# Kernel optimization log

Measured on AMD Instinct MI355X. Metric: run time of the kernel, lower is better.

The kernel has to match this reference:

```python
import jax, jax.numpy as jnp
import numpy as np
import math

EMB = 128
HW = 128

def setup_inputs() -> dict:
    key = jax.random.key(0)
    k_t, k1, k2, k3, k4 = jax.random.split(key, 5)
    B = 8192
    t = jax.random.uniform(k_t, (B,), dtype=jnp.float32)
    s = 1.0 / math.sqrt(EMB)
    W1 = jax.random.uniform(k1, (EMB, EMB), dtype=jnp.float32, minval=-s, maxval=s)
    b1 = jax.random.uniform(k2, (EMB,), dtype=jnp.float32, minval=-s, maxval=s)
    W2 = jax.random.uniform(k3, (EMB, EMB), dtype=jnp.float32, minval=-s, maxval=s)
    b2 = jax.random.uniform(k4, (EMB,), dtype=jnp.float32, minval=-s, maxval=s)
    return {"t": t, "W1": W1, "b1": b1, "W2": W2, "b2": b2}

def reference(t, W1, b1, W2, b2):
    # sinusoidal embedding: 64 log-spaced freqs in [1, 1000]
    freqs = jnp.exp(jnp.linspace(math.log(1.0), math.log(1000.0), EMB // 2)).astype(jnp.float32)
    ang = (2.0 * math.pi) * freqs  # [64]
    phase = t[:, None] * ang[None, :]  # [B, 64]
    emb = jnp.concatenate([jnp.sin(phase), jnp.cos(phase)], axis=-1)  # [B, 128]
    # MLP: Linear -> SiLU -> Linear -> SiLU (torch Linear: x @ W.T + b)
    h = jax.nn.silu(emb @ W1.T + b1)
    h = jax.nn.silu(h @ W2.T + b2)
    # [B,1,1,128] nearest-upsampled to [B,1,128,128]: broadcast along H
    out = jnp.broadcast_to(h[:, None, None, :], (h.shape[0], 1, HW, HW))
    return out
```

## Files before the change

### kernel.cpp

```cpp
#include <hip/hip_runtime.h>
#include <math.h>

typedef float f32x4 __attribute__((ext_vector_type(4)));

__global__ __launch_bounds__(256) void k_mlp(
    const float* __restrict__ t,
    const float* __restrict__ W1, const float* __restrict__ b1,
    const float* __restrict__ W2, const float* __restrict__ b2,
    float* __restrict__ hs)
{
    __shared__ __attribute__((aligned(16))) float emb[16][128];
    __shared__ __attribute__((aligned(16))) float h1[16][128];

    const int tid  = threadIdx.x;
    const int base = blockIdx.x * 16;

    #pragma unroll
    for (int i = 0; i < 4; ++i) {
        int idx = i * 256 + tid;
        int b   = idx >> 6;
        int k   = idx & 63;
        double a   = (double)k * (6.907755278982137 / 63.0);
        float freq = (float)exp(a);
        float ang  = 6.2831853071795865f * freq;
        float ph   = t[base + b] * ang;
        float sv, cv;
        sincosf(ph, &sv, &cv);
        emb[b][k]      = sv;
        emb[b][64 + k] = cv;
    }
    __syncthreads();

    const int jj   = tid & 127;
    const int half = tid >> 7;

    {
        float acc[8];
        float bv = b1[jj];
        #pragma unroll
        for (int m = 0; m < 8; ++m) acc[m] = bv;
        const float4* w = (const float4*)(W1 + jj * 128);
        #pragma unroll
        for (int k4 = 0; k4 < 32; ++k4) {
            float4 wv = w[k4];
            #pragma unroll
            for (int m = 0; m < 8; ++m) {
                float4 ev = ((const float4*)emb[half * 8 + m])[k4];
                acc[m] = fmaf(wv.x, ev.x, acc[m]);
                acc[m] = fmaf(wv.y, ev.y, acc[m]);
                acc[m] = fmaf(wv.z, ev.z, acc[m]);
                acc[m] = fmaf(wv.w, ev.w, acc[m]);
            }
        }
        #pragma unroll
        for (int m = 0; m < 8; ++m) {
            float a = acc[m];
            h1[half * 8 + m][jj] = a / (1.0f + expf(-a));
        }
    }
    __syncthreads();

    {
        float acc[8];
        float bv = b2[jj];
        #pragma unroll
        for (int m = 0; m < 8; ++m) acc[m] = bv;
        const float4* w = (const float4*)(W2 + jj * 128);
        #pragma unroll
        for (int k4 = 0; k4 < 32; ++k4) {
            float4 wv = w[k4];
            #pragma unroll
            for (int m = 0; m < 8; ++m) {
                float4 ev = ((const float4*)h1[half * 8 + m])[k4];
                acc[m] = fmaf(wv.x, ev.x, acc[m]);
                acc[m] = fmaf(wv.y, ev.y, acc[m]);
                acc[m] = fmaf(wv.z, ev.z, acc[m]);
                acc[m] = fmaf(wv.w, ev.w, acc[m]);
            }
        }
        #pragma unroll
        for (int m = 0; m < 8; ++m) {
            float a = acc[m];
            hs[(size_t)(base + half * 8 + m) * 128 + jj] = a / (1.0f + expf(-a));
        }
    }
}

__global__ __launch_bounds__(256) void k_bcast(
    const float* __restrict__ hs, float* __restrict__ out)
{
    const int tid = threadIdx.x;
    const size_t b = blockIdx.x;
    f32x4 v = ((const f32x4*)(hs + b * 128))[tid & 31];
    f32x4* d = (f32x4*)(out + b * 16384);
    #pragma unroll
    for (int c = 0; c < 16; ++c) {
        d[c * 256 + tid] = v;
    }
}

extern "C" void kernel_launch(void* const* d_in, const int* in_sizes, int n_in,
                              void* d_out, int out_size, void* d_ws, size_t ws_size,
                              hipStream_t stream) {
    const float* t  = (const float*)d_in[0];
    const float* W1 = (const float*)d_in[1];
    const float* b1 = (const float*)d_in[2];
    const float* W2 = (const float*)d_in[3];
    const float* b2 = (const float*)d_in[4];
    float* out = (float*)d_out;
    float* hs  = (float*)d_ws;
    const int B = in_sizes[0];

    k_mlp  <<<B / 16, 256, 0, stream>>>(t, W1, b1, W2, b2, hs);
    k_bcast<<<B,      256, 0, stream>>>(hs, out);
}
```

Measured before the change: 549.7 us.

## Fuse MLP and broadcast into one kernel with swizzled LDS-staged weights

Merges the MLP kernel and the broadcast kernel into a single kernel, so the intermediate hidden vectors stay in shared memory instead of making a round trip through a global workspace, and one launch is removed. Each block now handles 8 batch rows instead of 16. It stages each weight matrix transposed into a 64KB shared buffer using an XOR swizzle to avoid bank conflicts, replacing per-thread strided global weight reads. The cost is that every block reloads both 64KB weight matrices, and the large shared allocation limits occupancy. The output write of 512MB still dominates, and the fused kernel's store phase may now overlap less well with compute.

Result: no change. 543.2 us (-1.2%).

```diff
diff --git a/kernel.cpp b/kernel.cpp
--- a/kernel.cpp
+++ b/kernel.cpp
@@ -3,23 +3,41 @@
 
 typedef float f32x4 __attribute__((ext_vector_type(4)));
 
-__global__ __launch_bounds__(256) void k_mlp(
+__global__ __launch_bounds__(256) void k_fused(
     const float* __restrict__ t,
     const float* __restrict__ W1, const float* __restrict__ b1,
     const float* __restrict__ W2, const float* __restrict__ b2,
-    float* __restrict__ hs)
+    float* __restrict__ out)
 {
-    __shared__ __attribute__((aligned(16))) float emb[16][128];
-    __shared__ __attribute__((aligned(16))) float h1[16][128];
+    __shared__ float WL[128 * 128];
+    __shared__ __attribute__((aligned(16))) float emb[8][128];
+    __shared__ __attribute__((aligned(16))) float h1[8][128];
+    __shared__ __attribute__((aligned(16))) float h2[8][128];
 
     const int tid  = threadIdx.x;
-    const int base = blockIdx.x * 16;
+    const int base = blockIdx.x * 8;
+    const int jj   = tid & 127;
+    const int half = tid >> 7;
 
+    {
+        const f32x4* g = (const f32x4*)W1;
+        #pragma unroll
+        for (int it = 0; it < 16; ++it) {
+            int idx4 = it * 256 + tid;
+            f32x4 q = g[idx4];
+            int j  = idx4 >> 5;
+            int k0 = (idx4 & 31) * 4;
+            #pragma unroll
+            for (int i = 0; i < 4; ++i) {
+                int k = k0 + i;
+                WL[k * 128 + (j ^ (k & 31))] = q[i];
+            }
+        }
+    }
     #pragma unroll
-    for (int i = 0; i < 4; ++i) {
+    for (int i = 0; i < 2; ++i) {
         int idx = i * 256 + tid;
-        int b   = idx >> 6;
-        int k   = idx & 63;
+        int b = idx >> 6, k = idx & 63;
         double a   = (double)k * (6.907755278982137 / 63.0);
         float freq = (float)exp(a);
         float ang  = 6.2831853071795865f * freq;
@@ -31,71 +49,89 @@
     }
     __syncthreads();
 
-    const int jj   = tid & 127;
-    const int half = tid >> 7;
-
     {
-        float acc[8];
+        float acc[4];
         float bv = b1[jj];
         #pragma unroll
-        for (int m = 0; m < 8; ++m) acc[m] = bv;
-        const float4* w = (const float4*)(W1 + jj * 128);
+        for (int m = 0; m < 4; ++m) acc[m] = bv;
         #pragma unroll
         for (int k4 = 0; k4 < 32; ++k4) {
-            float4 wv = w[k4];
+            const int k0 = k4 * 4;
+            float w0 = WL[(k0 + 0) * 128 + (jj ^ ((k0 + 0) & 31))];
+            float w1 = WL[(k0 + 1) * 128 + (jj ^ ((k0 + 1) & 31))];
+            float w2 = WL[(k0 + 2) * 128 + (jj ^ ((k0 + 2) & 31))];
+            float w3 = WL[(k0 + 3) * 128 + (jj ^ ((k0 + 3) & 31))];
             #pragma unroll
-            for (int m = 0; m < 8; ++m) {
-                float4 ev = ((const float4*)emb[half * 8 + m])[k4];
-                acc[m] = fmaf(wv.x, ev.x, acc[m]);
-                acc[m] = fmaf(wv.y, ev.y, acc[m]);
-                acc[m] = fmaf(wv.z, ev.z, acc[m]);
-                acc[m] = fmaf(wv.w, ev.w, acc[m]);
+            for (int m = 0; m < 4; ++m) {
+                float4 ev = ((const float4*)emb[half * 4 + m])[k4];
+                acc[m] = fmaf(w0, ev.x, acc[m]);
+                acc[m] = fmaf(w1, ev.y, acc[m]);
+                acc[m] = fmaf(w2, ev.z, acc[m]);
+                acc[m] = fmaf(w3, ev.w, acc[m]);
             }
         }
         #pragma unroll
-        for (int m = 0; m < 8; ++m) {
+        for (int m = 0; m < 4; ++m) {
             float a = acc[m];
-            h1[half * 8 + m][jj] = a / (1.0f + expf(-a));
+            h1[half * 4 + m][jj] = a / (1.0f + expf(-a));
         }
     }
     __syncthreads();
 
     {
-        float acc[8];
+        const f32x4* g = (const f32x4*)W2;
+        #pragma unroll
+        for (int it = 0; it < 16; ++it) {
+            int idx4 = it * 256 + tid;
+            f32x4 q = g[idx4];
+            int j  = idx4 >> 5;
+            int k0 = (idx4 & 31) * 4;
+            #pragma unroll
+            for (int i = 0; i < 4; ++i) {
+                int k = k0 + i;
+                WL[k * 128 + (j ^ (k & 31))] = q[i];
+            }
+        }
+    }
+    __syncthreads();
+
+    {
+        float acc[4];
         float bv = b2[jj];
         #pragma unroll
-        for (int m = 0; m < 8; ++m) acc[m] = bv;
-        const float4* w = (const float4*)(W2 + jj * 128);
+        for (int m = 0; m < 4; ++m) acc[m] = bv;
         #pragma unroll
         for (int k4 = 0; k4 < 32; ++k4) {
-            float4 wv = w[k4];
+            const int k0 = k4 * 4;
+            float w0 = WL[(k0 + 0) * 128 + (jj ^ ((k0 + 0) & 31))];
+            float w1 = WL[(k0 + 1) * 128 + (jj ^ ((k0 + 1) & 31))];
+            float w2 = WL[(k0 + 2) * 128 + (jj ^ ((k0 + 2) & 31))];
+            float w3 = WL[(k0 + 3) * 128 + (jj ^ ((k0 + 3) & 31))];
             #pragma unroll
-            for (int m = 0; m < 8; ++m) {
-                float4 ev = ((const float4*)h1[half * 8 + m])[k4];
-                acc[m] = fmaf(wv.x, ev.x, acc[m]);
-                acc[m] = fmaf(wv.y, ev.y, acc[m]);
-                acc[m] = fmaf(wv.z, ev.z, acc[m]);
-                acc[m] = fmaf(wv.w, ev.w, acc[m]);
+            for (int m = 0; m < 4; ++m) {
+                float4 ev = ((const float4*)h1[half * 4 + m])[k4];
+                acc[m] = fmaf(w0, ev.x, acc[m]);
+                acc[m] = fmaf(w1, ev.y, acc[m]);
+                acc[m] = fmaf(w2, ev.z, acc[m]);
+                acc[m] = fmaf(w3, ev.w, acc[m]);
             }
         }
         #pragma unroll
-        for (int m = 0; m < 8; ++m) {
+        for (int m = 0; m < 4; ++m) {
             float a = acc[m];
-            hs[(size_t)(base + half * 8 + m) * 128 + jj] = a / (1.0f + expf(-a));
+            h2[half * 4 + m][jj] = a / (1.0f + expf(-a));
         }
     }
-}
+    __syncthreads();
 
-__global__ __launch_bounds__(256) void k_bcast(
-    const float* __restrict__ hs, float* __restrict__ out)
-{
-    const int tid = threadIdx.x;
-    const size_t b = blockIdx.x;
-    f32x4 v = ((const f32x4*)(hs + b * 128))[tid & 31];
-    f32x4* d = (f32x4*)(out + b * 16384);
     #pragma unroll
-    for (int c = 0; c < 16; ++c) {
-        d[c * 256 + tid] = v;
+    for (int m = 0; m < 8; ++m) {
+        f32x4 v = *(const f32x4*)&h2[m][(tid & 31) * 4];
+        f32x4* d = (f32x4*)(out + (size_t)(base + m) * 16384);
+        #pragma unroll
+        for (int c = 0; c < 16; ++c) {
+            d[c * 256 + tid] = v;
+        }
     }
 }
 
@@ -108,9 +144,7 @@
     const float* W2 = (const float*)d_in[3];
     const float* b2 = (const float*)d_in[4];
     float* out = (float*)d_out;
-    float* hs  = (float*)d_ws;
     const int B = in_sizes[0];
 
-    k_mlp  <<<B / 16, 256, 0, stream>>>(t, W1, b1, W2, b2, hs);
-    k_bcast<<<B,      256, 0, stream>>>(hs, out);
+    k_fused<<<B / 8, 256, 0, stream>>>(t, W1, b1, W2, b2, out);
 }
```
